# Optimization experiments

Measured on AMD Instinct MI355X. Metric: run time of the kernel, lower is better.

Reference implementation:

```python
import jax, jax.numpy as jnp
import numpy as np

EPS = 1e-5

def _conv(x, w, stride=1, pad=0, groups=1):
    return jax.lax.conv_general_dilated(x, w, (stride, stride), [(pad, pad), (pad, pad)],
                                        dimension_numbers=('NCHW', 'OIHW', 'NCHW'),
                                        feature_group_count=groups)

def _bn(x, g, b, m, v):
    # eval-mode BatchNorm2d with running stats
    return g[None, :, None, None] * (x - m[None, :, None, None]) / jnp.sqrt(v[None, :, None, None] + EPS) + b[None, :, None, None]

def setup_inputs():
    key = jax.random.key(0)
    ks = jax.random.split(key, 16)
    B, C, H = 32, 1024, 28
    G, Cg, Sq = 16, 64, 256  # groups, channels-per-group, SE squeeze width
    f32 = jnp.float32
    def bn_params(k):
        k1, k2, k3, k4 = jax.random.split(k, 4)
        return (jax.random.uniform(k1, (C,), f32, 0.5, 1.5),
                jax.random.normal(k2, (C,), f32) * 0.1,
                jax.random.normal(k3, (C,), f32) * 0.1,
                jax.random.uniform(k4, (C,), f32, 0.5, 1.5))
    ga, ba, ma, va = bn_params(ks[0])
    gb, bb, mb, vb = bn_params(ks[1])
    gc, bc, mc, vc = bn_params(ks[2])
    return dict(
        x=jax.random.normal(ks[3], (B, C, H, H), f32),
        temperature=1,
        wa=jax.random.normal(ks[4], (C, C, 1, 1), f32) * 0.03,
        ga=ga, ba=ba, ma=ma, va=va,
        wb=jax.random.normal(ks[5], (C, Cg, 3, 3), f32) * 0.04,
        gb=gb, bb=bb, mb=mb, vb=vb,
        sw1=jax.random.normal(ks[6], (Sq, C, 1, 1), f32) * 0.03, sb1=jnp.zeros((Sq,), f32),
        sw2=jax.random.normal(ks[7], (C, Sq, 1, 1), f32) * 0.06, sb2=jnp.zeros((C,), f32),
        wc=jax.random.normal(ks[8], (C, C, 1, 1), f32) * 0.03,
        gc=gc, bc=bc, mc=mc, vc=vc,
        mkw=jax.random.normal(ks[9], (2, C, 1, 1), f32) * 0.1,
        mkb=jnp.array([10.0, 0.0], f32) + jax.random.normal(ks[10], (2,), f32),
    )

def reference(x, temperature, wa, ga, ba, ma, va, wb, gb, bb, mb, vb,
              sw1, sb1, sw2, sb2, wc, gc, bc, mc, vc, mkw, mkb):
    B, C, H, W = x.shape
    ms = 7; r = H // ms; G = 16  # mask_size, upsample ratio, conv groups
    # ---- Masker (eval mode): adaptive avg-pool 28->7, 1x1 conv to 2 logit maps, hard select
    pooled = x.reshape(B, C, ms, r, ms, r).mean(axis=(3, 5))          # [B,C,7,7]
    logits = _conv(pooled, mkw) + mkb[None, :, None, None]            # [B,2,7,7]
    logits = logits.reshape(B, 2, 1, ms, ms)
    mask = (logits[:, 0] >= logits[:, 1]).astype(x.dtype)             # [B,1,7,7]
    sparsity = mask.mean()
    mask = jnp.repeat(jnp.repeat(mask, r, axis=2), r, axis=3)         # nearest upsample -> [B,1,28,28]
    # ExpandMask (stride=1): 3x3 all-ones conv, pad 1, threshold
    mask_dil = _conv(mask, jnp.ones((1, 1, 3, 3), x.dtype), pad=1) > 0.5
    sparsity_dil = mask_dil.astype(x.dtype).mean()
    mask_flops = C * ms * ms + (2 * C + C) * ms * ms  # as in source flops bookkeeping
    # ---- Bottleneck transform: 1x1 -> 3x3 grouped -> SE -> 1x1
    h = jax.nn.relu(_bn(_conv(x, wa), ga, ba, ma, va))
    h = jax.nn.relu(_bn(_conv(h, wb, pad=1, groups=G), gb, bb, mb, vb))
    s = h.mean(axis=(2, 3), keepdims=True)                            # SE squeeze
    s = jax.nn.relu(_conv(s, sw1) + sb1[None, :, None, None])
    s = jax.nn.sigmoid(_conv(s, sw2) + sb2[None, :, None, None])
    h = h * s
    h = _bn(_conv(h, wc), gc, bc, mc, vc)
    h = h * mask                                                      # apply_mask (g==1: broadcast)
    out = jax.nn.relu(h + x)                                          # identity residual (no proj)
    # ---- flops / sparsity bookkeeping (returned like the torch module)
    c1 = C * C; c2 = C * C * 9 // G; c3 = C * C
    dense = mask_flops + (c1 + c2 + c3) * H * W
    sparse = mask_flops + c1 * H * W * sparsity_dil + (c2 + c3) * H * W * sparsity
    perc = sparse / dense
    return (out, sparsity[None], sparsity_dil[None], perc[None], sparse)
```

## Files before the change

### kernel.cpp

```cpp
#include <hip/hip_runtime.h>

typedef __bf16 bf16;
typedef __bf16 bf16x8 __attribute__((ext_vector_type(8)));
typedef __bf16 bf16x4 __attribute__((ext_vector_type(4)));
typedef float  f32x4  __attribute__((ext_vector_type(4)));

#define EPSBN 1e-5f

__device__ __forceinline__ void gload16(const void* gp, void* lp) {
  __builtin_amdgcn_global_load_lds(
      (__attribute__((address_space(1))) void*)(unsigned long long)gp,
      (__attribute__((address_space(3))) void*)(unsigned)(unsigned long long)lp,
      16, 0, 0);
}

__global__ __launch_bounds__(256) void k_prep(
    const float* __restrict__ wa, const float* __restrict__ wc,
    const float* __restrict__ ga, const float* __restrict__ ba, const float* __restrict__ ma, const float* __restrict__ va,
    const float* __restrict__ gb, const float* __restrict__ bb, const float* __restrict__ mb, const float* __restrict__ vb,
    const float* __restrict__ gc, const float* __restrict__ bc, const float* __restrict__ mc, const float* __restrict__ vc,
    bf16* __restrict__ wa_bf, bf16* __restrict__ wc_bf, float* __restrict__ bn6,
    float* __restrict__ sums, unsigned* __restrict__ cnts)
{
  unsigned i = blockIdx.x * 256 + threadIdx.x;
  unsigned e = i * 4;
  float4 a = *(const float4*)(wa + e);
  bf16x4 av; av[0]=(bf16)a.x; av[1]=(bf16)a.y; av[2]=(bf16)a.z; av[3]=(bf16)a.w;
  *(bf16x4*)(wa_bf + e) = av;
  float4 c = *(const float4*)(wc + e);
  bf16x4 cv; cv[0]=(bf16)c.x; cv[1]=(bf16)c.y; cv[2]=(bf16)c.z; cv[3]=(bf16)c.w;
  *(bf16x4*)(wc_bf + e) = cv;
  if (i < 1024) {
    float s;
    s = ga[i] / sqrtf(va[i] + EPSBN); bn6[i]        = s; bn6[1024 + i] = ba[i] - ma[i] * s;
    s = gb[i] / sqrtf(vb[i] + EPSBN); bn6[2048 + i] = s; bn6[3072 + i] = bb[i] - mb[i] * s;
    s = gc[i] / sqrtf(vc[i] + EPSBN); bn6[4096 + i] = s; bn6[5120 + i] = bc[i] - mc[i] * s;
  }
  if (i < 32768) sums[i] = 0.f;
  if (i == 0) { cnts[0] = 0u; cnts[1] = 0u; }
}

__global__ __launch_bounds__(256) void k_prepw(const float* __restrict__ wb, bf16* __restrict__ wb_bf)
{
  int t = blockIdx.x * 256 + threadIdx.x;
  int ci = t & 63;
  int u  = t >> 6;
  int cl = u & 63;
  int gk = u >> 6;
  int g  = gk / 9, kk = gk - g * 9;
  wb_bf[t] = (bf16)wb[(((size_t)(g * 64 + cl) * 64) + ci) * 9 + kk];
}

__global__ __launch_bounds__(256) void k_ring(bf16* __restrict__ h1p)
{
  int t = blockIdx.x * 256 + threadIdx.x;
  int c8 = t & 127;
  int r  = (t >> 7) % 116;
  int b  = t / (116 * 128);
  int y, x;
  if (r < 30)      { y = 0;      x = r; }
  else if (r < 60) { y = 29;     x = r - 30; }
  else if (r < 88) { y = r - 59; x = 0; }
  else             { y = r - 87; x = 29; }
  size_t off = (((size_t)b * 30 + y) * 30 + x) * 1024 + (size_t)c8 * 8;
  *(uint4*)(h1p + off) = uint4{0, 0, 0, 0};
}

__global__ __launch_bounds__(256) void k_cast_pool(
    const float* __restrict__ x, bf16* __restrict__ xT, float* __restrict__ pooled)
{
  const int pt = blockIdx.x, ct = blockIdx.y, b = blockIdx.z;
  __shared__ float tile[64 * 116];
  const int tid = threadIdx.x;
  const float* src = x + ((size_t)(b * 1024 + ct * 64)) * 784 + pt * 112;
  #pragma unroll
  for (int it = 0; it < 7; it++) {
    unsigned f = tid + it * 256;
    unsigned ci = f / 28, j = f % 28;
    float4 v = *(const float4*)(src + (size_t)ci * 784 + j * 4);
    *(float4*)(tile + ci * 116 + j * 4) = v;
  }
  __syncthreads();
  bf16* dst = xT + ((size_t)(b * 784 + pt * 112)) * 1024 + ct * 64;
  for (int s = tid; s < 896; s += 256) {
    int j = s >> 3, c8 = s & 7;
    bf16x8 tmp;
    #pragma unroll
    for (int e = 0; e < 8; e++) tmp[e] = (bf16)tile[(c8 * 8 + e) * 116 + j];
    *(bf16x8*)(dst + (size_t)j * 1024 + c8 * 8) = tmp;
  }
  for (int s = tid; s < 448; s += 256) {
    int c = s / 7, ox = s % 7;
    float acc = 0.f;
    #pragma unroll
    for (int yy = 0; yy < 4; yy++)
      #pragma unroll
      for (int xx = 0; xx < 4; xx++)
        acc += tile[c * 116 + yy * 28 + ox * 4 + xx];
    pooled[((size_t)(b * 1024 + ct * 64 + c)) * 49 + pt * 7 + ox] = acc * (1.0f / 16.0f);
  }
}

__global__ __launch_bounds__(128) void k_mask(
    const float* __restrict__ pooled, const float* __restrict__ mkw, const float* __restrict__ mkb,
    float* __restrict__ mask7, unsigned* __restrict__ cnts)
{
  const int b = blockIdx.x, tid = threadIdx.x;
  __shared__ float l0s[49], l1s[49];
  __shared__ unsigned char m7[49];
  const int j = tid >> 6, p = tid & 63;
  if (p < 49) {
    const float* pb = pooled + (size_t)b * 1024 * 49 + p;
    const float* wr = mkw + j * 1024;
    float acc = 0.f;
    #pragma unroll 8
    for (int c = 0; c < 1024; c++) acc += pb[(size_t)c * 49] * wr[c];
    acc += mkb[j];
    if (j == 0) l0s[p] = acc; else l1s[p] = acc;
  }
  __syncthreads();
  if (tid < 49) {
    unsigned char m = (l0s[tid] >= l1s[tid]) ? 1 : 0;
    m7[tid] = m;
    mask7[b * 49 + tid] = (float)m;
  }
  __syncthreads();
  if (tid < 64) {
    unsigned long long bal = __ballot((tid < 49) && m7[tid]);
    if (tid == 0) atomicAdd(&cnts[0], (unsigned)__popcll(bal));
  }
  int cnt = 0;
  for (int p2 = tid; p2 < 784; p2 += 128) {
    int y = p2 / 28, x = p2 % 28;
    int cy0 = (y == 0) ? 0 : (y - 1) >> 2, cy1 = (y == 27) ? 6 : (y + 1) >> 2;
    int cx0 = (x == 0) ? 0 : (x - 1) >> 2, cx1 = (x == 27) ? 6 : (x + 1) >> 2;
    int d = 0;
    for (int cy = cy0; cy <= cy1; cy++)
      for (int cx = cx0; cx <= cx1; cx++) d |= m7[cy * 7 + cx];
    cnt += d;
  }
  cnt += __shfl_xor(cnt, 1);  cnt += __shfl_xor(cnt, 2);  cnt += __shfl_xor(cnt, 4);
  cnt += __shfl_xor(cnt, 8);  cnt += __shfl_xor(cnt, 16); cnt += __shfl_xor(cnt, 32);
  __shared__ int wsum[2];
  if ((tid & 63) == 0) wsum[tid >> 6] = cnt;
  __syncthreads();
  if (tid == 0) atomicAdd(&cnts[1], (unsigned)(wsum[0] + wsum[1]));
}

__global__ void k_fin(const unsigned* __restrict__ cnts, float* __restrict__ tail)
{
  if (threadIdx.x == 0 && blockIdx.x == 0) {
    float sp = (float)cnts[0] / 1568.0f;
    float sd = (float)cnts[1] / 25088.0f;
    const float c1 = 1048576.0f, c2 = 589824.0f, c3 = 1048576.0f, mf = 200704.0f;
    float dense  = mf + (c1 + c2 + c3) * 784.0f;
    float sparse = mf + c1 * 784.0f * sd + (c2 + c3) * 784.0f * sp;
    tail[0] = sp; tail[1] = sd; tail[2] = sparse / dense; tail[3] = sparse;
  }
}

template<int MODE>
__global__ __launch_bounds__(256) void k_gemm(
    const bf16* __restrict__ Aop, const bf16* __restrict__ Bop, void* __restrict__ outp,
    const float* __restrict__ bn6, const float* __restrict__ xres,
    const float* __restrict__ mask7, const float* __restrict__ s2)
{
  const int mt = (MODE == 0) ? blockIdx.x : blockIdx.y;
  const int nt = (MODE == 0) ? blockIdx.y : blockIdx.x;
  __shared__ bf16 ldsA[8192];
  __shared__ bf16 ldsB[8192];
  __shared__ float ldsS[MODE ? 2048 : 4];
  const int tid = threadIdx.x, lane = tid & 63, w = tid >> 6;
  const int wm = w & 1, wn = w >> 1;
  const int li = lane & 15, q = lane >> 4;

  int b0 = 0, soff[4];
  if constexpr (MODE == 1) {
    b0 = (mt * 128) / 784;
    int b1 = (mt * 128 + 127) / 784;
    for (int i = tid; i < 512; i += 256) {
      int bs = i >> 7, f4 = i & 127;
      *(f32x4*)(ldsS + i * 4) = *(const f32x4*)(s2 + (size_t)(bs ? b1 : b0) * 1024 + f4 * 4);
    }
    #pragma unroll
    for (int m = 0; m < 4; m++)
      soff[m] = (((mt * 128 + wm * 64 + m * 16) / 784) - b0) * 1024;
  }

  const bf16* Ab = Aop + (size_t)mt * 128 * 1024;
  const bf16* Bb = Bop + (size_t)nt * 128 * 1024;
  const bf16* ga[4]; const bf16* gb[4];
  #pragma unroll
  for (int j = 0; j < 4; j++) {
    int c = w * 256 + j * 64 + lane;
    int row = c >> 3, k8 = (c & 7) ^ (row & 7);
    ga[j] = Ab + (size_t)row * 1024 + k8 * 8;
    gb[j] = Bb + (size_t)row * 1024 + k8 * 8;
  }
  const int lb = li * 128 + ((q ^ (li & 7)) << 4);
  f32x4 acc[4][4] = {};

  for (int kt = 0; kt < 16; kt++) {
    #pragma unroll
    for (int j = 0; j < 4; j++) gload16(ga[j], (char*)ldsA + w * 4096 + j * 1024);
    #pragma unroll
    for (int j = 0; j < 4; j++) gload16(gb[j], (char*)ldsB + w * 4096 + j * 1024);
    #pragma unroll
    for (int j = 0; j < 4; j++) { ga[j] += 64; gb[j] += 64; }
    __syncthreads();
    #pragma unroll
    for (int ks = 0; ks < 2; ks++) {
      bf16x8 af[4], bfr[4];
      #pragma unroll
      for (int m = 0; m < 4; m++)
        af[m] = *(const bf16x8*)((const char*)ldsA + wm * 8192 + m * 2048 + (lb ^ (ks * 64)));
      #pragma unroll
      for (int n = 0; n < 4; n++)
        bfr[n] = *(const bf16x8*)((const char*)ldsB + wn * 8192 + n * 2048 + (lb ^ (ks * 64)));
      if constexpr (MODE == 1) {
        #pragma unroll
        for (int m = 0; m < 4; m++) {
          const float* sp = ldsS + soff[m] + kt * 64 + ks * 32 + q * 8;
          f32x4 s0 = *(const f32x4*)sp;
          f32x4 s1 = *(const f32x4*)(sp + 4);
          #pragma unroll
          for (int j = 0; j < 4; j++) {
            af[m][j]     = (bf16)((float)af[m][j]     * s0[j]);
            af[m][4 + j] = (bf16)((float)af[m][4 + j] * s1[j]);
          }
        }
      }
      #pragma unroll
      for (int m = 0; m < 4; m++)
        #pragma unroll
        for (int n = 0; n < 4; n++)
          acc[m][n] = __builtin_amdgcn_mfma_f32_16x16x32_bf16(af[m], bfr[n], acc[m][n], 0, 0, 0);
    }
    __syncthreads();
  }

  if constexpr (MODE == 0) {
    bf16* h1p = (bf16*)outp;
    const int co0 = mt * 128 + wm * 64 + q * 4;
    f32x4 sv[4], ov[4];
    #pragma unroll
    for (int m = 0; m < 4; m++) {
      sv[m] = *(const f32x4*)(bn6 + co0 + m * 16);
      ov[m] = *(const f32x4*)(bn6 + 1024 + co0 + m * 16);
    }
    #pragma unroll
    for (int n = 0; n < 4; n++) {
      unsigned p = nt * 128 + wn * 64 + n * 16 + li;
      unsigned b = p / 784u, rem = p % 784u;
      unsigned y = rem / 28u, xx = rem % 28u;
      bf16* dst = h1p + (((size_t)b * 30 + y + 1) * 30 + xx + 1) * 1024 + co0;
      #pragma unroll
      for (int m = 0; m < 4; m++) {
        bf16x4 pk;
        #pragma unroll
        for (int r = 0; r < 4; r++)
          pk[r] = (bf16)fmaxf(acc[m][n][r] * sv[m][r] + ov[m][r], 0.f);
        *(bf16x4*)(dst + m * 16) = pk;
      }
    }
  } else {
    float* dst = (float*)outp;
    const int p0 = mt * 128 + wm * 64 + q * 4;
    int bM[4]; unsigned hwM[4]; float mvv[4];
    #pragma unroll
    for (int m = 0; m < 4; m++) {
      int pm = p0 + m * 16;
      int b = pm / 784; unsigned hw = pm - b * 784;
      bM[m] = b; hwM[m] = hw;
      unsigned y = hw / 28u, xx = hw % 28u;
      mvv[m] = mask7[b * 49 + (y >> 2) * 7 + (xx >> 2)];
    }
    #pragma unroll
    for (int n = 0; n < 4; n++) {
      int co = nt * 128 + wn * 64 + n * 16 + li;
      float s = bn6[4096 + co], o = bn6[5120 + co];
      #pragma unroll
      for (int m = 0; m < 4; m++) {
        size_t base = ((size_t)(bM[m] * 1024 + co)) * 784 + hwM[m];
        f32x4 xv = *(const f32x4*)(xres + base);
        f32x4 rv;
        #pragma unroll
        for (int r = 0; r < 4; r++) {
          float v = acc[m][n][r] * s + o;
          rv[r] = fmaxf(v * mvv[m] + xv[r], 0.f);
        }
        *(f32x4*)(dst + base) = rv;
      }
    }
  }
}

__global__ __launch_bounds__(256) void k_conv_b(
    const bf16* __restrict__ h1p, const bf16* __restrict__ wb_bf,
    bf16* __restrict__ h2T, float* __restrict__ sums, const float* __restrict__ bn6)
{
  const int b = blockIdx.x, g = blockIdx.y, yt = blockIdx.z;
  __shared__ bf16 ldsI[184 * 64];
  const int tid = threadIdx.x, lane = tid & 63, w = tid >> 6;
  const int li = lane & 15, q = lane >> 4;

  bf16x8 wreg[9][2];
  #pragma unroll
  for (int kk = 0; kk < 9; kk++)
    #pragma unroll
    for (int cs = 0; cs < 2; cs++)
      wreg[kk][cs] = *(const bf16x8*)(wb_bf +
          (((size_t)(g * 9 + kk) * 64) + w * 16 + li) * 64 + cs * 32 + q * 8);

  const bf16* iBase = h1p + (size_t)b * 921600 + (size_t)(4 * yt) * 30 * 1024 + g * 64;
  #pragma unroll
  for (int t = 0; t < 6; t++) {
    int j = w + t * 4;
    if (j < 23 && (j < 22 || lane < 32)) {
      int c = j * 64 + lane;
      int pos = c >> 3, ci8 = (c & 7) ^ (pos & 7);
      gload16(iBase + (size_t)pos * 1024 + ci8 * 8, (char*)ldsI + j * 1024);
    }
  }

  int pos0[7];
  #pragma unroll
  for (int mtt = 0; mtt < 7; mtt++) {
    int n = mtt * 16 + li;
    pos0[mtt] = (n / 28) * 30 + (n % 28);
  }
  __syncthreads();

  f32x4 acc[7] = {};
  #pragma unroll
  for (int kk = 0; kk < 9; kk++) {
    const int shift = (kk / 3) * 30 + (kk % 3);
    #pragma unroll
    for (int cs = 0; cs < 2; cs++) {
      #pragma unroll
      for (int mtt = 0; mtt < 7; mtt++) {
        int pos = pos0[mtt] + shift;
        int off = pos * 128 + ((((cs << 2) + q) ^ (pos & 7)) << 4);
        bf16x8 ifr = *(const bf16x8*)((const char*)ldsI + off);
        acc[mtt] = __builtin_amdgcn_mfma_f32_16x16x32_bf16(wreg[kk][cs], ifr, acc[mtt], 0, 0, 0);
      }
    }
  }

  const int co4 = g * 64 + w * 16 + q * 4;
  f32x4 sv = *(const f32x4*)(bn6 + 2048 + co4);
  f32x4 ov = *(const f32x4*)(bn6 + 3072 + co4);
  f32x4 csum = {0.f, 0.f, 0.f, 0.f};
  #pragma unroll
  for (int mtt = 0; mtt < 7; mtt++) {
    int pl = yt * 112 + mtt * 16 + li;
    bf16x4 pk;
    #pragma unroll
    for (int r = 0; r < 4; r++) {
      float v = fmaxf(acc[mtt][r] * sv[r] + ov[r], 0.f);
      csum[r] += v;
      pk[r] = (bf16)v;
    }
    *(bf16x4*)(h2T + ((size_t)b * 784 + pl) * 1024 + co4) = pk;
  }
  #pragma unroll
  for (int d = 1; d < 16; d <<= 1) {
    #pragma unroll
    for (int r = 0; r < 4; r++) csum[r] += __shfl_xor(csum[r], d);
  }
  if (li == 0) {
    #pragma unroll
    for (int r = 0; r < 4; r++) atomicAdd(&sums[b * 1024 + co4 + r], csum[r]);
  }
}

__global__ __launch_bounds__(256) void k_se(
    const float* __restrict__ sums, const float* __restrict__ sw1, const float* __restrict__ sb1,
    const float* __restrict__ sw2, const float* __restrict__ sb2, float* __restrict__ s2)
{
  const int b = blockIdx.x, tid = threadIdx.x;
  __shared__ float mean[1024];
  __shared__ float s1[256];
  for (int i = tid; i < 1024; i += 256) mean[i] = sums[b * 1024 + i] * (1.0f / 784.0f);
  __syncthreads();
  {
    float acc = sb1[tid];
    const float4* wr = (const float4*)(sw1 + (size_t)tid * 1024);
    #pragma unroll 4
    for (int c4 = 0; c4 < 256; c4++) {
      float4 wv = wr[c4];
      acc += wv.x * mean[c4 * 4] + wv.y * mean[c4 * 4 + 1] + wv.z * mean[c4 * 4 + 2] + wv.w * mean[c4 * 4 + 3];
    }
    s1[tid] = fmaxf(acc, 0.f);
  }
  __syncthreads();
  for (int co = tid; co < 1024; co += 256) {
    float acc = sb2[co];
    const float4* wr = (const float4*)(sw2 + (size_t)co * 256);
    #pragma unroll 4
    for (int q4 = 0; q4 < 64; q4++) {
      float4 wv = wr[q4];
      acc += wv.x * s1[q4 * 4] + wv.y * s1[q4 * 4 + 1] + wv.z * s1[q4 * 4 + 2] + wv.w * s1[q4 * 4 + 3];
    }
    s2[b * 1024 + co] = 1.0f / (1.0f + __expf(-acc));
  }
}

extern "C" void kernel_launch(void* const* d_in, const int* in_sizes, int n_in,
                              void* d_out, int out_size, void* d_ws, size_t ws_size,
                              hipStream_t stream)
{
  const float* x   = (const float*)d_in[0];
  const float* wa  = (const float*)d_in[2];
  const float* ga  = (const float*)d_in[3];
  const float* ba  = (const float*)d_in[4];
  const float* ma  = (const float*)d_in[5];
  const float* va  = (const float*)d_in[6];
  const float* wb  = (const float*)d_in[7];
  const float* gb  = (const float*)d_in[8];
  const float* bb  = (const float*)d_in[9];
  const float* mb  = (const float*)d_in[10];
  const float* vb  = (const float*)d_in[11];
  const float* sw1 = (const float*)d_in[12];
  const float* sb1 = (const float*)d_in[13];
  const float* sw2 = (const float*)d_in[14];
  const float* sb2 = (const float*)d_in[15];
  const float* wc  = (const float*)d_in[16];
  const float* gc  = (const float*)d_in[17];
  const float* bc  = (const float*)d_in[18];
  const float* mc  = (const float*)d_in[19];
  const float* vc  = (const float*)d_in[20];
  const float* mkw = (const float*)d_in[21];
  const float* mkb = (const float*)d_in[22];

  char* ws = (char*)d_ws;
  bf16*  xT     = (bf16*)(ws + 0);
  bf16*  h1p    = (bf16*)(ws + 51380224);
  bf16*  wa_bf  = (bf16*)(ws + 110428160);
  bf16*  wc_bf  = (bf16*)(ws + 112525312);
  float* pooled = (float*)(ws + 114622464);
  bf16*  wb_bf  = (bf16*)(ws + 114622464);
  float* mask7  = (float*)(ws + 121044992);
  float* sums   = (float*)(ws + 121053184);
  float* s2     = (float*)(ws + 121184256);
  float* bn6    = (float*)(ws + 121315328);
  unsigned* cnts = (unsigned*)(ws + 121339904);

  float* out = (float*)d_out;

  k_prep<<<1024, 256, 0, stream>>>(wa, wc, ga, ba, ma, va, gb, bb, mb, vb, gc, bc, mc, vc,
                                   wa_bf, wc_bf, bn6, sums, cnts);
  k_ring<<<1856, 256, 0, stream>>>(h1p);
  k_cast_pool<<<dim3(7, 16, 32), 256, 0, stream>>>(x, xT, pooled);
  k_mask<<<32, 128, 0, stream>>>(pooled, mkw, mkb, mask7, cnts);
  k_fin<<<1, 64, 0, stream>>>(cnts, out + 25690112);
  k_prepw<<<2304, 256, 0, stream>>>(wb, wb_bf);
  k_gemm<0><<<dim3(8, 196), 256, 0, stream>>>(wa_bf, xT, h1p, bn6, nullptr, nullptr, nullptr);
  k_conv_b<<<dim3(32, 16, 7), 256, 0, stream>>>(h1p, wb_bf, xT , sums, bn6);
  k_se<<<32, 256, 0, stream>>>(sums, sw1, sb1, sw2, sb2, s2);
  k_gemm<1><<<dim3(8, 196), 256, 0, stream>>>(xT , wc_bf, out, bn6, x, mask7, s2);
}
```

Measured before the change: 617.9 us.

## Merge prep kernels, parallelize SE and mask, hoist SE scaling, remap GEMM grid

Folds the weight-cast, grouped-weight permute and halo-zeroing kernels into one init launch. The pooled map is stored channel-last in bf16 so the mask logits can be computed with coalesced wave reductions. The SE MLP is split into two wider-grid kernels, and the channel scaling moves out of the final GEMM's inner loop into a separate elementwise pass over h2. Both GEMMs use a 1D grid with a swizzled tile order meant to improve cache reuse. The extra scale pass costs one more read and write of the 51 MB activation, plus an extra rounding of h2 to bf16.

```diff
diff --git a/kernel.cpp b/kernel.cpp
--- a/kernel.cpp
+++ b/kernel.cpp
@@ -14,60 +14,58 @@
       16, 0, 0);
 }
 
-__global__ __launch_bounds__(256) void k_prep(
-    const float* __restrict__ wa, const float* __restrict__ wc,
+__global__ __launch_bounds__(256) void k_init(
+    const float* __restrict__ wa, const float* __restrict__ wc, const float* __restrict__ wb,
     const float* __restrict__ ga, const float* __restrict__ ba, const float* __restrict__ ma, const float* __restrict__ va,
     const float* __restrict__ gb, const float* __restrict__ bb, const float* __restrict__ mb, const float* __restrict__ vb,
     const float* __restrict__ gc, const float* __restrict__ bc, const float* __restrict__ mc, const float* __restrict__ vc,
-    bf16* __restrict__ wa_bf, bf16* __restrict__ wc_bf, float* __restrict__ bn6,
-    float* __restrict__ sums, unsigned* __restrict__ cnts)
-{
-  unsigned i = blockIdx.x * 256 + threadIdx.x;
-  unsigned e = i * 4;
-  float4 a = *(const float4*)(wa + e);
-  bf16x4 av; av[0]=(bf16)a.x; av[1]=(bf16)a.y; av[2]=(bf16)a.z; av[3]=(bf16)a.w;
-  *(bf16x4*)(wa_bf + e) = av;
-  float4 c = *(const float4*)(wc + e);
-  bf16x4 cv; cv[0]=(bf16)c.x; cv[1]=(bf16)c.y; cv[2]=(bf16)c.z; cv[3]=(bf16)c.w;
-  *(bf16x4*)(wc_bf + e) = cv;
-  if (i < 1024) {
-    float s;
-    s = ga[i] / sqrtf(va[i] + EPSBN); bn6[i]        = s; bn6[1024 + i] = ba[i] - ma[i] * s;
-    s = gb[i] / sqrtf(vb[i] + EPSBN); bn6[2048 + i] = s; bn6[3072 + i] = bb[i] - mb[i] * s;
-    s = gc[i] / sqrtf(vc[i] + EPSBN); bn6[4096 + i] = s; bn6[5120 + i] = bc[i] - mc[i] * s;
-  }
-  if (i < 32768) sums[i] = 0.f;
-  if (i == 0) { cnts[0] = 0u; cnts[1] = 0u; }
-}
-
-__global__ __launch_bounds__(256) void k_prepw(const float* __restrict__ wb, bf16* __restrict__ wb_bf)
-{
-  int t = blockIdx.x * 256 + threadIdx.x;
-  int ci = t & 63;
-  int u  = t >> 6;
-  int cl = u & 63;
-  int gk = u >> 6;
-  int g  = gk / 9, kk = gk - g * 9;
-  wb_bf[t] = (bf16)wb[(((size_t)(g * 64 + cl) * 64) + ci) * 9 + kk];
-}
-
-__global__ __launch_bounds__(256) void k_ring(bf16* __restrict__ h1p)
-{
-  int t = blockIdx.x * 256 + threadIdx.x;
-  int c8 = t & 127;
-  int r  = (t >> 7) % 116;
-  int b  = t / (116 * 128);
-  int y, x;
-  if (r < 30)      { y = 0;      x = r; }
-  else if (r < 60) { y = 29;     x = r - 30; }
-  else if (r < 88) { y = r - 59; x = 0; }
-  else             { y = r - 87; x = 29; }
-  size_t off = (((size_t)b * 30 + y) * 30 + x) * 1024 + (size_t)c8 * 8;
-  *(uint4*)(h1p + off) = uint4{0, 0, 0, 0};
+    bf16* __restrict__ wa_bf, bf16* __restrict__ wc_bf, bf16* __restrict__ wb_bf,
+    float* __restrict__ bn6, float* __restrict__ sums, unsigned* __restrict__ cnts,
+    bf16* __restrict__ h1p)
+{
+  const int bid = blockIdx.x, tid = threadIdx.x;
+  if (bid < 1024) {
+    unsigned i = bid * 256 + tid;
+    unsigned e = i * 4;
+    float4 a = *(const float4*)(wa + e);
+    bf16x4 av; av[0]=(bf16)a.x; av[1]=(bf16)a.y; av[2]=(bf16)a.z; av[3]=(bf16)a.w;
+    *(bf16x4*)(wa_bf + e) = av;
+    float4 c = *(const float4*)(wc + e);
+    bf16x4 cv; cv[0]=(bf16)c.x; cv[1]=(bf16)c.y; cv[2]=(bf16)c.z; cv[3]=(bf16)c.w;
+    *(bf16x4*)(wc_bf + e) = cv;
+    if (i < 1024) {
+      float s;
+      s = ga[i] / sqrtf(va[i] + EPSBN); bn6[i]        = s; bn6[1024 + i] = ba[i] - ma[i] * s;
+      s = gb[i] / sqrtf(vb[i] + EPSBN); bn6[2048 + i] = s; bn6[3072 + i] = bb[i] - mb[i] * s;
+      s = gc[i] / sqrtf(vc[i] + EPSBN); bn6[4096 + i] = s; bn6[5120 + i] = bc[i] - mc[i] * s;
+    }
+    if (i < 32768) sums[i] = 0.f;
+    if (i == 0) { cnts[0] = 0u; cnts[1] = 0u; }
+  } else if (bid < 3328) {
+    int t = (bid - 1024) * 256 + tid;
+    int ci = t & 63;
+    int u  = t >> 6;
+    int cl = u & 63;
+    int gk = u >> 6;
+    int g  = gk / 9, kk = gk - g * 9;
+    wb_bf[t] = (bf16)wb[(((size_t)(g * 64 + cl) * 64) + ci) * 9 + kk];
+  } else {
+    int t = (bid - 3328) * 256 + tid;
+    int c8 = t & 127;
+    int r  = (t >> 7) % 116;
+    int b  = t / (116 * 128);
+    int y, x;
+    if (r < 30)      { y = 0;      x = r; }
+    else if (r < 60) { y = 29;     x = r - 30; }
+    else if (r < 88) { y = r - 59; x = 0; }
+    else             { y = r - 87; x = 29; }
+    size_t off = (((size_t)b * 30 + y) * 30 + x) * 1024 + (size_t)c8 * 8;
+    *(uint4*)(h1p + off) = uint4{0, 0, 0, 0};
+  }
 }
 
 __global__ __launch_bounds__(256) void k_cast_pool(
-    const float* __restrict__ x, bf16* __restrict__ xT, float* __restrict__ pooled)
+    const float* __restrict__ x, bf16* __restrict__ xT, bf16* __restrict__ pooledb)
 {
   const int pt = blockIdx.x, ct = blockIdx.y, b = blockIdx.z;
   __shared__ float tile[64 * 116];
@@ -97,26 +95,39 @@
       #pragma unroll
       for (int xx = 0; xx < 4; xx++)
         acc += tile[c * 116 + yy * 28 + ox * 4 + xx];
-    pooled[((size_t)(b * 1024 + ct * 64 + c)) * 49 + pt * 7 + ox] = acc * (1.0f / 16.0f);
-  }
-}
-
-__global__ __launch_bounds__(128) void k_mask(
-    const float* __restrict__ pooled, const float* __restrict__ mkw, const float* __restrict__ mkb,
+    pooledb[((size_t)b * 49 + pt * 7 + ox) * 1024 + ct * 64 + c] = (bf16)(acc * (1.0f / 16.0f));
+  }
+}
+
+__global__ __launch_bounds__(256) void k_mask(
+    const bf16* __restrict__ pooledb, const float* __restrict__ mkw, const float* __restrict__ mkb,
     float* __restrict__ mask7, unsigned* __restrict__ cnts)
 {
   const int b = blockIdx.x, tid = threadIdx.x;
+  const int lane = tid & 63, w = tid >> 6;
   __shared__ float l0s[49], l1s[49];
-  __shared__ unsigned char m7[49];
-  const int j = tid >> 6, p = tid & 63;
-  if (p < 49) {
-    const float* pb = pooled + (size_t)b * 1024 * 49 + p;
-    const float* wr = mkw + j * 1024;
-    float acc = 0.f;
-    #pragma unroll 8
-    for (int c = 0; c < 1024; c++) acc += pb[(size_t)c * 49] * wr[c];
-    acc += mkb[j];
-    if (j == 0) l0s[p] = acc; else l1s[p] = acc;
+  __shared__ unsigned char m7[56];
+  float w0r[16], w1r[16];
+  #pragma unroll
+  for (int i = 0; i < 4; i++) {
+    *(f32x4*)(w0r + i * 4) = *(const f32x4*)(mkw + lane * 16 + i * 4);
+    *(f32x4*)(w1r + i * 4) = *(const f32x4*)(mkw + 1024 + lane * 16 + i * 4);
+  }
+  const float mkb0 = mkb[0], mkb1 = mkb[1];
+  for (int p = w; p < 49; p += 4) {
+    const bf16* pp = pooledb + ((size_t)b * 49 + p) * 1024 + lane * 16;
+    bf16x8 h0 = *(const bf16x8*)pp;
+    bf16x8 h1 = *(const bf16x8*)(pp + 8);
+    float a0 = 0.f, a1 = 0.f;
+    #pragma unroll
+    for (int e = 0; e < 8; e++) {
+      float v0 = (float)h0[e], v1 = (float)h1[e];
+      a0 += v0 * w0r[e] + v1 * w0r[8 + e];
+      a1 += v0 * w1r[e] + v1 * w1r[8 + e];
+    }
+    #pragma unroll
+    for (int d = 1; d < 64; d <<= 1) { a0 += __shfl_xor(a0, d); a1 += __shfl_xor(a1, d); }
+    if (lane == 0) { l0s[p] = a0 + mkb0; l1s[p] = a1 + mkb1; }
   }
   __syncthreads();
   if (tid < 49) {
@@ -130,7 +141,7 @@
     if (tid == 0) atomicAdd(&cnts[0], (unsigned)__popcll(bal));
   }
   int cnt = 0;
-  for (int p2 = tid; p2 < 784; p2 += 128) {
+  for (int p2 = tid; p2 < 784; p2 += 256) {
     int y = p2 / 28, x = p2 % 28;
     int cy0 = (y == 0) ? 0 : (y - 1) >> 2, cy1 = (y == 27) ? 6 : (y + 1) >> 2;
     int cx0 = (x == 0) ? 0 : (x - 1) >> 2, cx1 = (x == 27) ? 6 : (x + 1) >> 2;
@@ -139,12 +150,12 @@
       for (int cx = cx0; cx <= cx1; cx++) d |= m7[cy * 7 + cx];
     cnt += d;
   }
-  cnt += __shfl_xor(cnt, 1);  cnt += __shfl_xor(cnt, 2);  cnt += __shfl_xor(cnt, 4);
-  cnt += __shfl_xor(cnt, 8);  cnt += __shfl_xor(cnt, 16); cnt += __shfl_xor(cnt, 32);
-  __shared__ int wsum[2];
-  if ((tid & 63) == 0) wsum[tid >> 6] = cnt;
-  __syncthreads();
-  if (tid == 0) atomicAdd(&cnts[1], (unsigned)(wsum[0] + wsum[1]));
+  #pragma unroll
+  for (int d = 1; d < 64; d <<= 1) cnt += __shfl_xor(cnt, d);
+  __shared__ int wsum[4];
+  if (lane == 0) wsum[w] = cnt;
+  __syncthreads();
+  if (tid == 0) atomicAdd(&cnts[1], (unsigned)(wsum[0] + wsum[1] + wsum[2] + wsum[3]));
 }
 
 __global__ void k_fin(const unsigned* __restrict__ cnts, float* __restrict__ tail)
@@ -163,29 +174,19 @@
 __global__ __launch_bounds__(256) void k_gemm(
     const bf16* __restrict__ Aop, const bf16* __restrict__ Bop, void* __restrict__ outp,
     const float* __restrict__ bn6, const float* __restrict__ xres,
-    const float* __restrict__ mask7, const float* __restrict__ s2)
-{
-  const int mt = (MODE == 0) ? blockIdx.x : blockIdx.y;
-  const int nt = (MODE == 0) ? blockIdx.y : blockIdx.x;
+    const float* __restrict__ mask7)
+{
+  int id = blockIdx.x, pixt, cot;
+  if (id < 1536) { pixt = (id >> 6) * 8 + (id & 7); cot = (id >> 3) & 7; }
+  else { int wi = id - 1536; pixt = 192 + (wi & 3); cot = wi >> 2; }
+  const int mt = (MODE == 0) ? cot : pixt;
+  const int nt = (MODE == 0) ? pixt : cot;
+
   __shared__ bf16 ldsA[8192];
   __shared__ bf16 ldsB[8192];
-  __shared__ float ldsS[MODE ? 2048 : 4];
   const int tid = threadIdx.x, lane = tid & 63, w = tid >> 6;
   const int wm = w & 1, wn = w >> 1;
   const int li = lane & 15, q = lane >> 4;
-
-  int b0 = 0, soff[4];
-  if constexpr (MODE == 1) {
-    b0 = (mt * 128) / 784;
-    int b1 = (mt * 128 + 127) / 784;
-    for (int i = tid; i < 512; i += 256) {
-      int bs = i >> 7, f4 = i & 127;
-      *(f32x4*)(ldsS + i * 4) = *(const f32x4*)(s2 + (size_t)(bs ? b1 : b0) * 1024 + f4 * 4);
-    }
-    #pragma unroll
-    for (int m = 0; m < 4; m++)
-      soff[m] = (((mt * 128 + wm * 64 + m * 16) / 784) - b0) * 1024;
-  }
 
   const bf16* Ab = Aop + (size_t)mt * 128 * 1024;
   const bf16* Bb = Bop + (size_t)nt * 128 * 1024;
@@ -217,19 +218,6 @@
       #pragma unroll
       for (int n = 0; n < 4; n++)
         bfr[n] = *(const bf16x8*)((const char*)ldsB + wn * 8192 + n * 2048 + (lb ^ (ks * 64)));
-      if constexpr (MODE == 1) {
-        #pragma unroll
-        for (int m = 0; m < 4; m++) {
-          const float* sp = ldsS + soff[m] + kt * 64 + ks * 32 + q * 8;
-          f32x4 s0 = *(const f32x4*)sp;
-          f32x4 s1 = *(const f32x4*)(sp + 4);
-          #pragma unroll
-          for (int j = 0; j < 4; j++) {
-            af[m][j]     = (bf16)((float)af[m][j]     * s0[j]);
-            af[m][4 + j] = (bf16)((float)af[m][4 + j] * s1[j]);
-          }
-        }
-      }
       #pragma unroll
       for (int m = 0; m < 4; m++)
         #pragma unroll
@@ -374,36 +362,56 @@
   }
 }
 
-__global__ __launch_bounds__(256) void k_se(
+__global__ __launch_bounds__(256) void k_se1(
     const float* __restrict__ sums, const float* __restrict__ sw1, const float* __restrict__ sb1,
-    const float* __restrict__ sw2, const float* __restrict__ sb2, float* __restrict__ s2)
-{
-  const int b = blockIdx.x, tid = threadIdx.x;
+    float* __restrict__ s1g)
+{
+  const int sqc = blockIdx.x, b = blockIdx.y, tid = threadIdx.x;
   __shared__ float mean[1024];
-  __shared__ float s1[256];
   for (int i = tid; i < 1024; i += 256) mean[i] = sums[b * 1024 + i] * (1.0f / 784.0f);
   __syncthreads();
-  {
-    float acc = sb1[tid];
-    const float4* wr = (const float4*)(sw1 + (size_t)tid * 1024);
-    #pragma unroll 4
-    for (int c4 = 0; c4 < 256; c4++) {
-      float4 wv = wr[c4];
-      acc += wv.x * mean[c4 * 4] + wv.y * mean[c4 * 4 + 1] + wv.z * mean[c4 * 4 + 2] + wv.w * mean[c4 * 4 + 3];
-    }
-    s1[tid] = fmaxf(acc, 0.f);
-  }
-  __syncthreads();
-  for (int co = tid; co < 1024; co += 256) {
-    float acc = sb2[co];
-    const float4* wr = (const float4*)(sw2 + (size_t)co * 256);
-    #pragma unroll 4
-    for (int q4 = 0; q4 < 64; q4++) {
-      float4 wv = wr[q4];
-      acc += wv.x * s1[q4 * 4] + wv.y * s1[q4 * 4 + 1] + wv.z * s1[q4 * 4 + 2] + wv.w * s1[q4 * 4 + 3];
-    }
-    s2[b * 1024 + co] = 1.0f / (1.0f + __expf(-acc));
-  }
+  const int row = sqc * 32 + (tid >> 3), part = tid & 7;
+  const f32x4* wr = (const f32x4*)(sw1 + (size_t)row * 1024 + part * 128);
+  const float* mr = mean + part * 128;
+  float acc = 0.f;
+  #pragma unroll 8
+  for (int i = 0; i < 32; i++) {
+    f32x4 wv = wr[i];
+    acc += wv[0] * mr[i * 4] + wv[1] * mr[i * 4 + 1] + wv[2] * mr[i * 4 + 2] + wv[3] * mr[i * 4 + 3];
+  }
+  acc += __shfl_xor(acc, 1); acc += __shfl_xor(acc, 2); acc += __shfl_xor(acc, 4);
+  if (part == 0) s1g[b * 256 + row] = fmaxf(acc + sb1[row], 0.f);
+}
+
+__global__ __launch_bounds__(256) void k_se2(
+    const float* __restrict__ s1g, const float* __restrict__ sw2, const float* __restrict__ sb2,
+    float* __restrict__ s2)
+{
+  const int coc = blockIdx.x, b = blockIdx.y, tid = threadIdx.x;
+  __shared__ float s1s[256];
+  s1s[tid] = s1g[b * 256 + tid];
+  __syncthreads();
+  const int co = coc * 256 + tid;
+  const f32x4* wr = (const f32x4*)(sw2 + (size_t)co * 256);
+  float acc = sb2[co];
+  #pragma unroll 8
+  for (int i = 0; i < 64; i++) {
+    f32x4 wv = wr[i];
+    acc += wv[0] * s1s[i * 4] + wv[1] * s1s[i * 4 + 1] + wv[2] * s1s[i * 4 + 2] + wv[3] * s1s[i * 4 + 3];
+  }
+  s2[b * 1024 + co] = 1.0f / (1.0f + __expf(-acc));
+}
+
+__global__ __launch_bounds__(256) void k_scale(bf16* __restrict__ h2T, const float* __restrict__ s2)
+{
+  size_t idx = ((size_t)blockIdx.x * 256 + threadIdx.x) * 8;
+  unsigned b = (unsigned)(idx / 802816u);
+  unsigned c = (unsigned)(idx & 1023u);
+  const float* sp = s2 + b * 1024 + c;
+  bf16x8 v = *(const bf16x8*)(h2T + idx);
+  #pragma unroll
+  for (int e = 0; e < 8; e++) v[e] = (bf16)((float)v[e] * sp[e]);
+  *(bf16x8*)(h2T + idx) = v;
 }
 
 extern "C" void kernel_launch(void* const* d_in, const int* in_sizes, int n_in,
@@ -434,29 +442,30 @@
   const float* mkb = (const float*)d_in[22];
 
   char* ws = (char*)d_ws;
-  bf16*  xT     = (bf16*)(ws + 0);
-  bf16*  h1p    = (bf16*)(ws + 51380224);
-  bf16*  wa_bf  = (bf16*)(ws + 110428160);
-  bf16*  wc_bf  = (bf16*)(ws + 112525312);
-  float* pooled = (float*)(ws + 114622464);
-  bf16*  wb_bf  = (bf16*)(ws + 114622464);
-  float* mask7  = (float*)(ws + 121044992);
-  float* sums   = (float*)(ws + 121053184);
-  float* s2     = (float*)(ws + 121184256);
-  float* bn6    = (float*)(ws + 121315328);
-  unsigned* cnts = (unsigned*)(ws + 121339904);
+  bf16*  xT      = (bf16*)(ws + 0);
+  bf16*  h1p     = (bf16*)(ws + 51380224);
+  bf16*  wa_bf   = (bf16*)(ws + 110362624);
+  bf16*  wc_bf   = (bf16*)(ws + 112459776);
+  bf16*  wb_bf   = (bf16*)(ws + 114556928);
+  bf16*  pooledb = (bf16*)(ws + 115736576);
+  float* mask7   = (float*)(ws + 118947840);
+  float* sums    = (float*)(ws + 118956032);
+  float* s1g     = (float*)(ws + 119087104);
+  float* s2      = (float*)(ws + 119119872);
+  float* bn6     = (float*)(ws + 119250944);
+  unsigned* cnts = (unsigned*)(ws + 119275520);
 
   float* out = (float*)d_out;
 
-  k_prep<<<1024, 256, 0, stream>>>(wa, wc, ga, ba, ma, va, gb, bb, mb, vb, gc, bc, mc, vc,
-                                   wa_bf, wc_bf, bn6, sums, cnts);
-  k_ring<<<1856, 256, 0, stream>>>(h1p);
-  k_cast_pool<<<dim3(7, 16, 32), 256, 0, stream>>>(x, xT, pooled);
-  k_mask<<<32, 128, 0, stream>>>(pooled, mkw, mkb, mask7, cnts);
+  k_init<<<5184, 256, 0, stream>>>(wa, wc, wb, ga, ba, ma, va, gb, bb, mb, vb, gc, bc, mc, vc,
+                                   wa_bf, wc_bf, wb_bf, bn6, sums, cnts, h1p);
+  k_cast_pool<<<dim3(7, 16, 32), 256, 0, stream>>>(x, xT, pooledb);
+  k_mask<<<32, 256, 0, stream>>>(pooledb, mkw, mkb, mask7, cnts);
   k_fin<<<1, 64, 0, stream>>>(cnts, out + 25690112);
-  k_prepw<<<2304, 256, 0, stream>>>(wb, wb_bf);
-  k_gemm<0><<<dim3(8, 196), 256, 0, stream>>>(wa_bf, xT, h1p, bn6, nullptr, nullptr, nullptr);
+  k_gemm<0><<<1568, 256, 0, stream>>>(wa_bf, xT, h1p, bn6, nullptr, nullptr);
   k_conv_b<<<dim3(32, 16, 7), 256, 0, stream>>>(h1p, wb_bf, xT , sums, bn6);
-  k_se<<<32, 256, 0, stream>>>(sums, sw1, sb1, sw2, sb2, s2);
-  k_gemm<1><<<dim3(8, 196), 256, 0, stream>>>(xT , wc_bf, out, bn6, x, mask7, s2);
-}
+  k_se1<<<dim3(8, 32), 256, 0, stream>>>(sums, sw1, sb1, s1g);
+  k_se2<<<dim3(4, 32), 256, 0, stream>>>(s1g, sw2, sb2, s2);
+  k_scale<<<12544, 256, 0, stream>>>(xT, s2);
+  k_gemm<1><<<1568, 256, 0, stream>>>(xT , wc_bf, out, bn6, x, mask7);
+}
```

After: 502.0 us. 1.23x faster.
